# Optimization experiments

Hardware: AMD Instinct MI355X
Metric: run time of the kernel (lower is better)

Reference implementation:

```python
import jax, jax.numpy as jnp
import numpy as np
import math

B, T, D, H = 4, 1024, 1024, 16
HD = D // H  # 64
ROPE_BASE = 10000.0


def _apply_rope(q, k):
    # q, k: [B, H, T, HD]; interleaved even/odd rotation as in RotaryEmbedding
    t_len = q.shape[2]
    half = q.shape[-1] // 2
    inv_freq = 1.0 / (ROPE_BASE ** (jnp.arange(half, dtype=jnp.float32) / half))
    freqs = jnp.arange(t_len, dtype=jnp.float32)[:, None] * inv_freq  # [T, half]
    cos = jnp.cos(freqs)
    sin = jnp.sin(freqs)

    def rot(u):
        u1 = u[..., ::2]   # even lanes
        u2 = u[..., 1::2]  # odd lanes
        e = u1 * cos - u2 * sin
        o = u2 * cos + u1 * sin
        return jnp.stack([e, o], axis=-1).reshape(u.shape)

    return rot(q), rot(k)


def _split_heads(x):
    b, t, d = x.shape
    return x.reshape(b, t, H, HD).transpose(0, 2, 1, 3)  # [B,H,T,HD]


def _mha(x, Wq, bq, Wk, bk, Wv, bv, Wo, bo, mask):
    q = _split_heads(jnp.einsum('btd,ed->bte', x, Wq) + bq)
    k = _split_heads(jnp.einsum('btd,ed->bte', x, Wk) + bk)
    v = _split_heads(jnp.einsum('btd,ed->bte', x, Wv) + bv)
    q, k = _apply_rope(q, k)
    scores = jnp.einsum('bhtd,bhsd->bhts', q.astype(jnp.float32),
                        k.astype(jnp.float32)) / math.sqrt(HD)
    scores = jnp.where(mask, scores, -jnp.inf)
    attn = jax.nn.softmax(scores, axis=-1).astype(v.dtype)
    ctx = jnp.einsum('bhts,bhsd->bhtd', attn.astype(jnp.float32),
                     v.astype(jnp.float32)).astype(v.dtype)
    ctx = ctx.transpose(0, 2, 1, 3).reshape(x.shape[0], x.shape[1], D)
    z = jnp.einsum('btd,ed->bte', ctx, Wo) + bo
    return z


def setup_inputs() -> dict:
    key = jax.random.key(0)
    ks = jax.random.split(key, 9)
    s = 0.02
    inp = {
        'x':  jax.random.normal(ks[0], (B, T, D), jnp.float32),
        'Wq': jax.random.normal(ks[1], (D, D), jnp.float32) * s,
        'bq': jax.random.normal(ks[2], (D,), jnp.float32) * s,
        'Wk': jax.random.normal(ks[3], (D, D), jnp.float32) * s,
        'bk': jax.random.normal(ks[4], (D,), jnp.float32) * s,
        'Wv': jax.random.normal(ks[5], (D, D), jnp.float32) * s,
        'bv': jax.random.normal(ks[6], (D,), jnp.float32) * s,
        'Wo': jax.random.normal(ks[7], (D, D), jnp.float32) * s,
        'bo': jax.random.normal(ks[8], (D,), jnp.float32) * s,
        'mask': jnp.tril(jnp.ones((T, T), dtype=bool))[None, None],  # causal
    }
    return inp


def reference(x, Wq, bq, Wk, bk, Wv, bv, Wo, bo, mask):
    return _mha(x, Wq, bq, Wk, bk, Wv, bv, Wo, bo, mask)
```

## Files before the change

### kernel.cpp

```cpp
#include <hip/hip_runtime.h>


#define T_SEQ 1024
#define NH    16
#define HDIM  64
#define DM    1024
#define MTOK  4096

typedef __attribute__((ext_vector_type(8))) short short8;
typedef __attribute__((ext_vector_type(4))) float f32x4;
typedef unsigned short u16;

__device__ __forceinline__ u16 f2bf(float f) {
  unsigned int u = __builtin_bit_cast(unsigned int, f);
  u += 0x7fffu + ((u >> 16) & 1u);
  return (u16)(u >> 16);
}

__device__ __forceinline__ void gll16(const void* g, void* l) {
  __builtin_amdgcn_global_load_lds(
      (const __attribute__((address_space(1))) unsigned int*)(unsigned long long)(g),
      (__attribute__((address_space(3))) unsigned int*)(unsigned int)(unsigned long long)(l),
      16, 0, 0);
}

__global__ void cvt4(const float* __restrict__ in, u16* __restrict__ out) {
  int i = blockIdx.x * 256 + threadIdx.x;
  float4 f = ((const float4*)in)[i];
  unsigned long long pk = (unsigned long long)f2bf(f.x)
                        | ((unsigned long long)f2bf(f.y) << 16)
                        | ((unsigned long long)f2bf(f.z) << 32)
                        | ((unsigned long long)f2bf(f.w) << 48);
  ((unsigned long long*)out)[i] = pk;
}

__global__ void cvtW(const float* __restrict__ w0, const float* __restrict__ w1,
                     const float* __restrict__ w2, const float* __restrict__ w3,
                     u16* __restrict__ out) {
  const float* src = blockIdx.y == 0 ? w0 : blockIdx.y == 1 ? w1 : blockIdx.y == 2 ? w2 : w3;
  u16* dst = out + (size_t)blockIdx.y * (DM * DM);
  int i = blockIdx.x * 256 + threadIdx.x;
  float4 f = ((const float4*)src)[i];
  unsigned long long pk = (unsigned long long)f2bf(f.x)
                        | ((unsigned long long)f2bf(f.y) << 16)
                        | ((unsigned long long)f2bf(f.z) << 32)
                        | ((unsigned long long)f2bf(f.w) << 48);
  ((unsigned long long*)dst)[i] = pk;
}

__global__ void rope_tab(float* __restrict__ c, float* __restrict__ s) {
  int idx = blockIdx.x * 256 + threadIdx.x;
  int t = idx >> 5, i = idx & 31;
  float inv = powf(10000.f, -(float)i * (1.0f / 32.0f));
  float f = (float)t * inv;
  c[idx] = cosf(f);
  s[idx] = sinf(f);
}

__device__ __forceinline__ void gemm_mainloop(
    const u16* __restrict__ A, const u16* __restrict__ Bw,
    int m0, int n0, int K, u16* Asm, u16* Bsm, f32x4 acc[4][4]) {
  const int tid = threadIdx.x, lane = tid & 63, wave = tid >> 6;
  const int wr = wave >> 1, wc = wave & 1;
  for (int k0 = 0; k0 < K; k0 += 32) {
#pragma unroll
    for (int c = 0; c < 2; ++c) {
      gll16(&A[(size_t)(m0 + c * 64 + (tid >> 2)) * K + k0 + (tid & 3) * 8], &Asm[c * 2048 + tid * 8]);
      gll16(&Bw[(size_t)(n0 + c * 64 + (tid >> 2)) * K + k0 + (tid & 3) * 8], &Bsm[c * 2048 + tid * 8]);
    }
    __syncthreads();
    short8 af[4], bf[4];
#pragma unroll
    for (int i = 0; i < 4; ++i) {
      af[i] = *(const short8*)&Asm[(wr * 64 + i * 16 + (lane & 15)) * 32 + ((lane >> 4) * 8)];
      bf[i] = *(const short8*)&Bsm[(wc * 64 + i * 16 + (lane & 15)) * 32 + ((lane >> 4) * 8)];
    }
#pragma unroll
    for (int i = 0; i < 4; ++i)
#pragma unroll
      for (int j = 0; j < 4; ++j)
        acc[i][j] = __builtin_amdgcn_mfma_f32_16x16x32_bf16(af[i], bf[j], acc[i][j], 0, 0, 0);
    __syncthreads();
  }
}

__global__ __launch_bounds__(256) void qkv_kernel(
    const u16* __restrict__ xb,
    const u16* __restrict__ Wqb, const u16* __restrict__ Wkb, const u16* __restrict__ Wvb,
    const float* __restrict__ bq, const float* __restrict__ bk, const float* __restrict__ bv,
    const float* __restrict__ ctab, const float* __restrict__ stab,
    u16* __restrict__ qbuf, u16* __restrict__ kbuf, u16* __restrict__ vt) {
  __shared__ __align__(16) u16 Asm[128 * 32];
  __shared__ __align__(16) u16 Bsm[128 * 32];
  const int mode = blockIdx.z;
  const u16* Bw = mode == 0 ? Wqb : (mode == 1 ? Wkb : Wvb);
  const float* bias = mode == 0 ? bq : (mode == 1 ? bk : bv);
  const int m0 = blockIdx.y * 128, n0 = blockIdx.x * 128;
  f32x4 acc[4][4];
#pragma unroll
  for (int i = 0; i < 4; ++i)
#pragma unroll
    for (int j = 0; j < 4; ++j)
#pragma unroll
      for (int r = 0; r < 4; ++r) acc[i][j][r] = 0.f;
  gemm_mainloop(xb, Bw, m0, n0, DM, Asm, Bsm, acc);

  const int lane = threadIdx.x & 63, wave = threadIdx.x >> 6;
  const int wr = wave >> 1, wc = wave & 1;
#pragma unroll
  for (int i = 0; i < 4; ++i) {
#pragma unroll
    for (int j = 0; j < 4; ++j) {
      const int e = n0 + wc * 64 + j * 16 + (lane & 15);
      const float bval = bias[e];
      const int h = e >> 6, hd = e & 63;
#pragma unroll
      for (int r = 0; r < 4; ++r) {
        const int m = m0 + wr * 64 + i * 16 + ((lane >> 4) * 4) + r;
        const int b = m >> 10, t = m & 1023;
        float v = acc[i][j][r] + bval;
        if (mode < 2) {
          float p = __shfl_xor(v, 1);
          const int fi = hd >> 1;
          const float cc = ctab[t * 32 + fi], ss = stab[t * 32 + fi];
          v = (hd & 1) ? (v * cc + p * ss) : (v * cc - p * ss);
          u16* dst = mode == 0 ? qbuf : kbuf;
          dst[(((size_t)(b * NH + h) * T_SEQ + t) << 6) + hd] = f2bf(v);
        } else {
          vt[(((size_t)(b * NH + h) * HDIM + hd) << 10) + t] = f2bf(v);
        }
      }
    }
  }
}

__global__ __launch_bounds__(256) void attn_kernel(
    const u16* __restrict__ qbuf, const u16* __restrict__ kbuf,
    const u16* __restrict__ vtb, u16* __restrict__ ctx) {
  __shared__ __align__(16) u16 Ks[2][64 * 64];
  __shared__ __align__(16) u16 Vs[2][64 * 64];
  __shared__ __align__(16) u16 Psm[4][16 * 64];
  const int bh = blockIdx.x;
  const int b = bh >> 4, h = bh & 15;
  const int tid = threadIdx.x, lane = tid & 63, wave = tid >> 6;
  const u16* Qp = qbuf + (size_t)bh * T_SEQ * HDIM;
  const u16* Kp = kbuf + (size_t)bh * T_SEQ * HDIM;
  const u16* Vp = vtb + (size_t)bh * HDIM * T_SEQ;
  u16* Pw = &Psm[wave][0];

  const int srow = tid >> 3;
  const int schx = ((tid & 7) ^ (srow & 7)) * 8;
  const int lx = lane & 7;

#define STG(kvt, bb)                                                            \
  do {                                                                          \
    _Pragma("unroll") for (int c = 0; c < 2; ++c) {                             \
      const int rr = c * 32 + srow;                                             \
      gll16(&Kp[(kvt) * 4096 + rr * 64 + schx], &Ks[bb][c * 2048 + tid * 8]);   \
      gll16(&Vp[(size_t)rr * T_SEQ + (kvt) * 64 + schx], &Vs[bb][c * 2048 + tid * 8]); \
    }                                                                           \
  } while (0)

  for (int phase = 0; phase < 2; ++phase) {
    const int qt = phase ? (15 - (int)blockIdx.y) : (int)blockIdx.y;
    const int q0 = qt * 64;
    const int nkv = qt + 1;
    const int qrow = q0 + wave * 16 + (lane & 15);
    const short8 qf0 = *(const short8*)&Qp[qrow * 64 + ((lane >> 4) * 8)];
    const short8 qf1 = *(const short8*)&Qp[qrow * 64 + 32 + ((lane >> 4) * 8)];

    f32x4 acc_o[4];
    float m_r[4], l_r[4];
#pragma unroll
    for (int i = 0; i < 4; ++i) {
#pragma unroll
      for (int r = 0; r < 4; ++r) acc_o[i][r] = 0.f;
      m_r[i] = -__builtin_inff();
      l_r[i] = 0.f;
    }

    __syncthreads();
    STG(0, 0);
    int cur = 0;

    for (int kvt = 0; kvt < nkv; ++kvt) {
      __syncthreads();
      if (kvt + 1 < nkv) STG(kvt + 1, cur ^ 1);

      f32x4 sacc[4];
#pragma unroll
      for (int cb = 0; cb < 4; ++cb) {
#pragma unroll
        for (int r = 0; r < 4; ++r) sacc[cb][r] = 0.f;
        const int krow = cb * 16 + (lane & 15);
        const short8 kf0 = *(const short8*)&Ks[cur][krow * 64 + (((lane >> 4) ^ lx) * 8)];
        const short8 kf1 = *(const short8*)&Ks[cur][krow * 64 + (((4 + (lane >> 4)) ^ lx) * 8)];
        sacc[cb] = __builtin_amdgcn_mfma_f32_16x16x32_bf16(qf0, kf0, sacc[cb], 0, 0, 0);
        sacc[cb] = __builtin_amdgcn_mfma_f32_16x16x32_bf16(qf1, kf1, sacc[cb], 0, 0, 0);
      }
      const int trow_base = q0 + wave * 16 + ((lane >> 4) * 4);
#pragma unroll
      for (int cb = 0; cb < 4; ++cb) {
        const int scol = kvt * 64 + cb * 16 + (lane & 15);
#pragma unroll
        for (int r = 0; r < 4; ++r) {
          float sv = sacc[cb][r] * 0.125f;
          sacc[cb][r] = (scol > trow_base + r) ? -__builtin_inff() : sv;
        }
      }
      float mt[4];
#pragma unroll
      for (int r = 0; r < 4; ++r)
        mt[r] = fmaxf(fmaxf(sacc[0][r], sacc[1][r]), fmaxf(sacc[2][r], sacc[3][r]));
#pragma unroll
      for (int off = 1; off < 16; off <<= 1)
#pragma unroll
        for (int r = 0; r < 4; ++r) mt[r] = fmaxf(mt[r], __shfl_xor(mt[r], off));
      float sf[4], lt[4];
#pragma unroll
      for (int r = 0; r < 4; ++r) {
        const float mn = fmaxf(m_r[r], mt[r]);
        sf[r] = __expf(m_r[r] - mn);
        m_r[r] = mn;
        lt[r] = 0.f;
      }
#pragma unroll
      for (int cb = 0; cb < 4; ++cb)
#pragma unroll
        for (int r = 0; r < 4; ++r) {
          const float p = __expf(sacc[cb][r] - m_r[r]);
          sacc[cb][r] = p;
          lt[r] += p;
        }
#pragma unroll
      for (int off = 1; off < 16; off <<= 1)
#pragma unroll
        for (int r = 0; r < 4; ++r) lt[r] += __shfl_xor(lt[r], off);
#pragma unroll
      for (int r = 0; r < 4; ++r) l_r[r] = l_r[r] * sf[r] + lt[r];
#pragma unroll
      for (int hb = 0; hb < 4; ++hb)
#pragma unroll
        for (int r = 0; r < 4; ++r) acc_o[hb][r] *= sf[r];

#pragma unroll
      for (int cb = 0; cb < 4; ++cb)
#pragma unroll
        for (int r = 0; r < 4; ++r) {
          const int prow = (lane >> 4) * 4 + r;
          Pw[prow * 64 + ((cb * 16 + (lane & 15)) ^ ((prow & 7) << 3))] = f2bf(sacc[cb][r]);
        }

      const int prr = lane & 15;
#pragma unroll
      for (int kc = 0; kc < 2; ++kc) {
        const short8 pf = *(const short8*)&Pw[prr * 64 + (((kc * 4 + (lane >> 4)) ^ lx) * 8)];
#pragma unroll
        for (int hb = 0; hb < 4; ++hb) {
          const int vrow = hb * 16 + (lane & 15);
          const short8 vf = *(const short8*)&Vs[cur][vrow * 64 + (((kc * 4 + (lane >> 4)) ^ lx) * 8)];
          acc_o[hb] = __builtin_amdgcn_mfma_f32_16x16x32_bf16(pf, vf, acc_o[hb], 0, 0, 0);
        }
      }
      cur ^= 1;
    }

#pragma unroll
    for (int hb = 0; hb < 4; ++hb) {
      const int hd = hb * 16 + (lane & 15);
#pragma unroll
      for (int r = 0; r < 4; ++r) {
        const int t = q0 + wave * 16 + ((lane >> 4) * 4) + r;
        const float v = acc_o[hb][r] / l_r[r];
        ctx[((size_t)(b * T_SEQ + t) * NH + h) * HDIM + hd] = f2bf(v);
      }
    }
  }
#undef STG
}

__global__ __launch_bounds__(256) void oproj_kernel(
    const u16* __restrict__ ctx, const u16* __restrict__ Wob,
    const float* __restrict__ bo, float* __restrict__ out) {
  __shared__ __align__(16) u16 Asm[128 * 32];
  __shared__ __align__(16) u16 Bsm[128 * 32];
  const int m0 = blockIdx.y * 128, n0 = blockIdx.x * 128;
  f32x4 acc[4][4];
#pragma unroll
  for (int i = 0; i < 4; ++i)
#pragma unroll
    for (int j = 0; j < 4; ++j)
#pragma unroll
      for (int r = 0; r < 4; ++r) acc[i][j][r] = 0.f;
  gemm_mainloop(ctx, Wob, m0, n0, DM, Asm, Bsm, acc);
  const int lane = threadIdx.x & 63, wave = threadIdx.x >> 6;
  const int wr = wave >> 1, wc = wave & 1;
#pragma unroll
  for (int i = 0; i < 4; ++i)
#pragma unroll
    for (int j = 0; j < 4; ++j) {
      const int e = n0 + wc * 64 + j * 16 + (lane & 15);
      const float bval = bo[e];
#pragma unroll
      for (int r = 0; r < 4; ++r) {
        const int m = m0 + wr * 64 + i * 16 + ((lane >> 4) * 4) + r;
        out[(size_t)m * DM + e] = acc[i][j][r] + bval;
      }
    }
}

extern "C" void kernel_launch(void* const* d_in, const int* in_sizes, int n_in,
                              void* d_out, int out_size, void* d_ws, size_t ws_size,
                              hipStream_t stream) {
  const float* x  = (const float*)d_in[0];
  const float* Wq = (const float*)d_in[1];
  const float* bq = (const float*)d_in[2];
  const float* Wk = (const float*)d_in[3];
  const float* bk = (const float*)d_in[4];
  const float* Wv = (const float*)d_in[5];
  const float* bv = (const float*)d_in[6];
  const float* Wo = (const float*)d_in[7];
  const float* bo = (const float*)d_in[8];

  char* w = (char*)d_ws;
  u16* xb   = (u16*)(w);
  u16* wqb  = (u16*)(w + (8ull << 20));
  u16* wkb  = (u16*)(w + (10ull << 20));
  u16* wvb  = (u16*)(w + (12ull << 20));
  u16* wob  = (u16*)(w + (14ull << 20));
  u16* qb   = (u16*)(w + (16ull << 20));
  u16* kb   = (u16*)(w + (24ull << 20));
  u16* vtb  = (u16*)(w + (32ull << 20));
  u16* ctxb = (u16*)(w + (40ull << 20));
  float* ctab = (float*)(w + (48ull << 20));
  float* stab = ctab + T_SEQ * 32;

  cvt4<<<dim3((MTOK * DM) / 4 / 256), 256, 0, stream>>>(x, xb);
  cvtW<<<dim3((DM * DM) / 4 / 256, 4), 256, 0, stream>>>(Wq, Wk, Wv, Wo, wqb);
  rope_tab<<<dim3((T_SEQ * 32) / 256), 256, 0, stream>>>(ctab, stab);
  qkv_kernel<<<dim3(DM / 128, MTOK / 128, 3), 256, 0, stream>>>(
      xb, wqb, wkb, wvb, bq, bk, bv, ctab, stab, qb, kb, vtb);
  attn_kernel<<<dim3(64, 8), 256, 0, stream>>>(qb, kb, vtb, ctxb);
  oproj_kernel<<<dim3(DM / 128, MTOK / 128), 256, 0, stream>>>(ctxb, wob, bo, (float*)d_out);
}
```

Measured before the change: 123.4 us.

## Triple-buffer GEMM mainloop with swizzled LDS and fuse prep kernels

Replaces the synchronous GEMM mainloop with a three-stage LDS ring. Global-to-LDS loads are issued two tiles ahead and gated by vmcnt waits, so load latency overlaps the MFMA work. LDS columns are XOR-swizzled to cut bank conflicts on fragment reads. The three conversion/rope-table launches are merged into one prep kernel, and the Q/K/V projections become one wide GEMM over contiguous weights with a 2D grid. The cost is triple the LDS per block, which may lower occupancy, and hand-written waitcnt/barrier logic that must be exactly right.

```diff
diff --git a/kernel.cpp b/kernel.cpp
--- a/kernel.cpp
+++ b/kernel.cpp
@@ -24,78 +24,102 @@
       16, 0, 0);
 }
 
-__global__ void cvt4(const float* __restrict__ in, u16* __restrict__ out) {
-  int i = blockIdx.x * 256 + threadIdx.x;
-  float4 f = ((const float4*)in)[i];
-  unsigned long long pk = (unsigned long long)f2bf(f.x)
-                        | ((unsigned long long)f2bf(f.y) << 16)
-                        | ((unsigned long long)f2bf(f.z) << 32)
-                        | ((unsigned long long)f2bf(f.w) << 48);
-  ((unsigned long long*)out)[i] = pk;
-}
-
-__global__ void cvtW(const float* __restrict__ w0, const float* __restrict__ w1,
-                     const float* __restrict__ w2, const float* __restrict__ w3,
-                     u16* __restrict__ out) {
-  const float* src = blockIdx.y == 0 ? w0 : blockIdx.y == 1 ? w1 : blockIdx.y == 2 ? w2 : w3;
-  u16* dst = out + (size_t)blockIdx.y * (DM * DM);
-  int i = blockIdx.x * 256 + threadIdx.x;
-  float4 f = ((const float4*)src)[i];
-  unsigned long long pk = (unsigned long long)f2bf(f.x)
-                        | ((unsigned long long)f2bf(f.y) << 16)
-                        | ((unsigned long long)f2bf(f.z) << 32)
-                        | ((unsigned long long)f2bf(f.w) << 48);
-  ((unsigned long long*)dst)[i] = pk;
-}
-
-__global__ void rope_tab(float* __restrict__ c, float* __restrict__ s) {
-  int idx = blockIdx.x * 256 + threadIdx.x;
-  int t = idx >> 5, i = idx & 31;
-  float inv = powf(10000.f, -(float)i * (1.0f / 32.0f));
-  float f = (float)t * inv;
-  c[idx] = cosf(f);
-  s[idx] = sinf(f);
-}
-
-__device__ __forceinline__ void gemm_mainloop(
+__global__ void prep_kernel(const float* __restrict__ x,
+                            const float* __restrict__ Wq, const float* __restrict__ Wk,
+                            const float* __restrict__ Wv, const float* __restrict__ Wo,
+                            u16* __restrict__ xb, u16* __restrict__ wall,
+                            float* __restrict__ ctab, float* __restrict__ stab) {
+  const int bid = blockIdx.x, tid = threadIdx.x;
+  if (bid < 8192) {
+    const float* src;
+    u16* dst;
+    int i;
+    if (bid < 4096) {
+      src = x; dst = xb; i = bid * 256 + tid;
+    } else {
+      const int w = (bid - 4096) >> 10;
+      src = w == 0 ? Wq : w == 1 ? Wk : w == 2 ? Wv : Wo;
+      dst = wall + (size_t)w * (DM * DM);
+      i = ((bid - 4096) & 1023) * 256 + tid;
+    }
+    float4 f = ((const float4*)src)[i];
+    unsigned long long pk = (unsigned long long)f2bf(f.x)
+                          | ((unsigned long long)f2bf(f.y) << 16)
+                          | ((unsigned long long)f2bf(f.z) << 32)
+                          | ((unsigned long long)f2bf(f.w) << 48);
+    ((unsigned long long*)dst)[i] = pk;
+  } else {
+    const int idx = (bid - 8192) * 256 + tid;
+    const int t = idx >> 5, i = idx & 31;
+    float inv = powf(10000.f, -(float)i * (1.0f / 32.0f));
+    float f = (float)t * inv;
+    ctab[idx] = cosf(f);
+    stab[idx] = sinf(f);
+  }
+}
+
+__device__ __forceinline__ void gemm_pipe(
     const u16* __restrict__ A, const u16* __restrict__ Bw,
-    int m0, int n0, int K, u16* Asm, u16* Bsm, f32x4 acc[4][4]) {
+    int m0, int n0, u16* As, u16* Bs, f32x4 acc[4][4]) {
   const int tid = threadIdx.x, lane = tid & 63, wave = tid >> 6;
   const int wr = wave >> 1, wc = wave & 1;
-  for (int k0 = 0; k0 < K; k0 += 32) {
-#pragma unroll
-    for (int c = 0; c < 2; ++c) {
-      gll16(&A[(size_t)(m0 + c * 64 + (tid >> 2)) * K + k0 + (tid & 3) * 8], &Asm[c * 2048 + tid * 8]);
-      gll16(&Bw[(size_t)(n0 + c * 64 + (tid >> 2)) * K + k0 + (tid & 3) * 8], &Bsm[c * 2048 + tid * 8]);
-    }
-    __syncthreads();
+  const int swz = ((tid & 3) ^ ((tid >> 3) & 3)) * 8;
+  const size_t Aofs = (size_t)(m0 + (tid >> 2)) * DM + swz;
+  const size_t Bofs = (size_t)(n0 + (tid >> 2)) * DM + swz;
+  const int ldst = tid * 8;
+  const int NT = DM / 32;
+
+#define STAGE_T(t, b)                                                   \
+  do {                                                                  \
+    gll16(&A[Aofs + (t) * 32],         &As[(b) * 4096 + ldst]);         \
+    gll16(&A[Aofs + 65536 + (t) * 32], &As[(b) * 4096 + 2048 + ldst]);  \
+    gll16(&Bw[Bofs + (t) * 32],        &Bs[(b) * 4096 + ldst]);         \
+    gll16(&Bw[Bofs + 65536 + (t) * 32], &Bs[(b) * 4096 + 2048 + ldst]); \
+  } while (0)
+
+  STAGE_T(0, 0);
+  STAGE_T(1, 1);
+  const int arow = (wr * 64 + (lane & 15)) * 32 + (((lane >> 4) ^ ((lane >> 1) & 3)) * 8);
+  const int brow = (wc * 64 + (lane & 15)) * 32 + (((lane >> 4) ^ ((lane >> 1) & 3)) * 8);
+  int cbuf = 0, sbuf = 2;
+  for (int t = 0; t < NT; ++t) {
+    if (t + 1 < NT) {
+      asm volatile("s_waitcnt vmcnt(4)" ::: "memory");
+    } else {
+      asm volatile("s_waitcnt vmcnt(0)" ::: "memory");
+    }
+    asm volatile("s_barrier" ::: "memory");
+    if (t + 2 < NT) STAGE_T(t + 2, sbuf);
     short8 af[4], bf[4];
 #pragma unroll
     for (int i = 0; i < 4; ++i) {
-      af[i] = *(const short8*)&Asm[(wr * 64 + i * 16 + (lane & 15)) * 32 + ((lane >> 4) * 8)];
-      bf[i] = *(const short8*)&Bsm[(wc * 64 + i * 16 + (lane & 15)) * 32 + ((lane >> 4) * 8)];
+      af[i] = *(const short8*)&As[cbuf * 4096 + arow + i * 512];
+      bf[i] = *(const short8*)&Bs[cbuf * 4096 + brow + i * 512];
     }
 #pragma unroll
     for (int i = 0; i < 4; ++i)
 #pragma unroll
       for (int j = 0; j < 4; ++j)
         acc[i][j] = __builtin_amdgcn_mfma_f32_16x16x32_bf16(af[i], bf[j], acc[i][j], 0, 0, 0);
-    __syncthreads();
+    asm volatile("s_waitcnt lgkmcnt(0)" ::: "memory");
+    asm volatile("s_barrier" ::: "memory");
+    cbuf = cbuf == 2 ? 0 : cbuf + 1;
+    sbuf = sbuf == 2 ? 0 : sbuf + 1;
   }
+#undef STAGE_T
 }
 
 __global__ __launch_bounds__(256) void qkv_kernel(
-    const u16* __restrict__ xb,
-    const u16* __restrict__ Wqb, const u16* __restrict__ Wkb, const u16* __restrict__ Wvb,
+    const u16* __restrict__ xb, const u16* __restrict__ wqkv,
     const float* __restrict__ bq, const float* __restrict__ bk, const float* __restrict__ bv,
     const float* __restrict__ ctab, const float* __restrict__ stab,
     u16* __restrict__ qbuf, u16* __restrict__ kbuf, u16* __restrict__ vt) {
-  __shared__ __align__(16) u16 Asm[128 * 32];
-  __shared__ __align__(16) u16 Bsm[128 * 32];
-  const int mode = blockIdx.z;
-  const u16* Bw = mode == 0 ? Wqb : (mode == 1 ? Wkb : Wvb);
+  __shared__ __align__(16) u16 As[3 * 4096];
+  __shared__ __align__(16) u16 Bs[3 * 4096];
+  const int m0 = blockIdx.y * 128;
+  const int n0 = blockIdx.x * 128;
+  const int mode = n0 >> 10;
   const float* bias = mode == 0 ? bq : (mode == 1 ? bk : bv);
-  const int m0 = blockIdx.y * 128, n0 = blockIdx.x * 128;
   f32x4 acc[4][4];
 #pragma unroll
   for (int i = 0; i < 4; ++i)
@@ -103,7 +127,7 @@
     for (int j = 0; j < 4; ++j)
 #pragma unroll
       for (int r = 0; r < 4; ++r) acc[i][j][r] = 0.f;
-  gemm_mainloop(xb, Bw, m0, n0, DM, Asm, Bsm, acc);
+  gemm_pipe(xb, wqkv, m0, n0, As, Bs, acc);
 
   const int lane = threadIdx.x & 63, wave = threadIdx.x >> 6;
   const int wr = wave >> 1, wc = wave & 1;
@@ -112,8 +136,8 @@
 #pragma unroll
     for (int j = 0; j < 4; ++j) {
       const int e = n0 + wc * 64 + j * 16 + (lane & 15);
-      const float bval = bias[e];
-      const int h = e >> 6, hd = e & 63;
+      const float bval = bias[e & 1023];
+      const int h = (e >> 6) & 15, hd = e & 63;
 #pragma unroll
       for (int r = 0; r < 4; ++r) {
         const int m = m0 + wr * 64 + i * 16 + ((lane >> 4) * 4) + r;
@@ -282,8 +306,8 @@
 __global__ __launch_bounds__(256) void oproj_kernel(
     const u16* __restrict__ ctx, const u16* __restrict__ Wob,
     const float* __restrict__ bo, float* __restrict__ out) {
-  __shared__ __align__(16) u16 Asm[128 * 32];
-  __shared__ __align__(16) u16 Bsm[128 * 32];
+  __shared__ __align__(16) u16 As[3 * 4096];
+  __shared__ __align__(16) u16 Bs[3 * 4096];
   const int m0 = blockIdx.y * 128, n0 = blockIdx.x * 128;
   f32x4 acc[4][4];
 #pragma unroll
@@ -292,7 +316,7 @@
     for (int j = 0; j < 4; ++j)
 #pragma unroll
       for (int r = 0; r < 4; ++r) acc[i][j][r] = 0.f;
-  gemm_mainloop(ctx, Wob, m0, n0, DM, Asm, Bsm, acc);
+  gemm_pipe(ctx, Wob, m0, n0, As, Bs, acc);
   const int lane = threadIdx.x & 63, wave = threadIdx.x >> 6;
   const int wr = wave >> 1, wc = wave & 1;
 #pragma unroll
@@ -324,9 +348,7 @@
 
   char* w = (char*)d_ws;
   u16* xb   = (u16*)(w);
-  u16* wqb  = (u16*)(w + (8ull << 20));
-  u16* wkb  = (u16*)(w + (10ull << 20));
-  u16* wvb  = (u16*)(w + (12ull << 20));
+  u16* wall = (u16*)(w + (8ull << 20));
   u16* wob  = (u16*)(w + (14ull << 20));
   u16* qb   = (u16*)(w + (16ull << 20));
   u16* kb   = (u16*)(w + (24ull << 20));
@@ -335,11 +357,9 @@
   float* ctab = (float*)(w + (48ull << 20));
   float* stab = ctab + T_SEQ * 32;
 
-  cvt4<<<dim3((MTOK * DM) / 4 / 256), 256, 0, stream>>>(x, xb);
-  cvtW<<<dim3((DM * DM) / 4 / 256, 4), 256, 0, stream>>>(Wq, Wk, Wv, Wo, wqb);
-  rope_tab<<<dim3((T_SEQ * 32) / 256), 256, 0, stream>>>(ctab, stab);
-  qkv_kernel<<<dim3(DM / 128, MTOK / 128, 3), 256, 0, stream>>>(
-      xb, wqb, wkb, wvb, bq, bk, bv, ctab, stab, qb, kb, vtb);
+  prep_kernel<<<dim3(8192 + 128), 256, 0, stream>>>(x, Wq, Wk, Wv, Wo, xb, wall, ctab, stab);
+  qkv_kernel<<<dim3(3 * DM / 128, MTOK / 128), 256, 0, stream>>>(
+      xb, wall, bq, bk, bv, ctab, stab, qb, kb, vtb);
   attn_kernel<<<dim3(64, 8), 256, 0, stream>>>(qb, kb, vtb, ctxb);
   oproj_kernel<<<dim3(DM / 128, MTOK / 128), 256, 0, stream>>>(ctxb, wob, bo, (float*)d_out);
 }
```

Result: faster. 116.1 us (-5.9%).
